# Optimization experiments

Measured on AMD Instinct MI355X. Metric: run time of the kernel, lower is better.

The kernel has to match this reference:

```python
import jax, jax.numpy as jnp
import numpy as np

DIM = 1024; N_LAYERS = 4; N_HEADS = 16; HEAD_DIM = DIM // N_HEADS
HIDDEN = 2816; VOCAB = 256; EPS = 1e-5; THETA = 10000.0
B, S = 1, 2048


def _rmsnorm(x, w):
    xf = x.astype(jnp.float32)
    n = xf * jax.lax.rsqrt(jnp.mean(xf * xf, axis=-1, keepdims=True) + EPS)
    return n.astype(x.dtype) * w


def _rope(x, cos, sin):
    # x: [B,S,H,hd]; torch view_as_complex pairs consecutive elements (0,1),(2,3),...
    xr = x[..., 0::2].astype(jnp.float32)
    xi = x[..., 1::2].astype(jnp.float32)
    c = cos[None, :, None, :]
    s = sin[None, :, None, :]
    outr = xr * c - xi * s
    outi = xr * s + xi * c
    out = jnp.stack([outr, outi], axis=-1).reshape(x.shape)
    return out.astype(x.dtype)


def setup_inputs() -> dict:
    key = jax.random.key(0)
    ks = jax.random.split(key, 10)
    std = 0.02
    def w(k, shape):
        return jax.random.normal(k, shape, jnp.float32) * std
    return {
        "tokens": jax.random.randint(ks[0], (B, S), 0, VOCAB, dtype=jnp.int32),
        "tok_emb": w(ks[1], (VOCAB, DIM)),
        "wq": w(ks[2], (N_LAYERS, DIM, DIM)),
        "wk": w(ks[3], (N_LAYERS, DIM, DIM)),
        "wv": w(ks[4], (N_LAYERS, DIM, DIM)),
        "wo": w(ks[5], (N_LAYERS, DIM, DIM)),
        "w1": w(ks[6], (N_LAYERS, HIDDEN, DIM)),
        "w2": w(ks[7], (N_LAYERS, DIM, HIDDEN)),
        "w3": w(ks[8], (N_LAYERS, HIDDEN, DIM)),
        "attn_norm_w": jnp.ones((N_LAYERS, DIM), jnp.float32),
        "ffn_norm_w": jnp.ones((N_LAYERS, DIM), jnp.float32),
        "final_norm_w": jnp.ones((DIM,), jnp.float32),
        "out_w": w(ks[9], (VOCAB, DIM)),
    }


def reference(tokens, tok_emb, wq, wk, wv, wo, w1, w2, w3,
              attn_norm_w, ffn_norm_w, final_norm_w, out_w):
    seqlen = tokens.shape[1]
    # precompute_freqs_cis
    inv = 1.0 / (THETA ** (jnp.arange(0, HEAD_DIM, 2, dtype=jnp.float32) / HEAD_DIM))
    t = jnp.arange(seqlen, dtype=jnp.float32)
    freqs = jnp.outer(t, inv)          # [S, hd/2]
    cos, sin = jnp.cos(freqs), jnp.sin(freqs)
    scale = 1.0 / np.sqrt(HEAD_DIM)

    h = tok_emb[tokens]                # [B,S,D]

    def block(h, p):
        lwq, lwk, lwv, lwo, lw1, lw2, lw3, anw, fnw = p
        x = _rmsnorm(h, anw)
        q = (x @ lwq.T).reshape(B, seqlen, N_HEADS, HEAD_DIM)
        k = (x @ lwk.T).reshape(B, seqlen, N_HEADS, HEAD_DIM)
        v = (x @ lwv.T).reshape(B, seqlen, N_HEADS, HEAD_DIM)
        q = _rope(q, cos, sin)
        k = _rope(k, cos, sin)
        # non-causal full attention (eval mode: no diffusion mask, no dropout)
        scores = jnp.einsum('bqhd,bkhd->bhqk', q, k) * scale
        probs = jax.nn.softmax(scores, axis=-1)
        attn = jnp.einsum('bhqk,bkhd->bqhd', probs, v).reshape(B, seqlen, DIM)
        h = h + attn @ lwo.T
        x = _rmsnorm(h, fnw)
        ff = (jax.nn.silu(x @ lw1.T) * (x @ lw3.T)) @ lw2.T
        return h + ff, None

    h, _ = jax.lax.scan(block, h, (wq, wk, wv, wo, w1, w2, w3, attn_norm_w, ffn_norm_w))
    h = _rmsnorm(h, final_norm_w)
    # targets=None path: logits only for the last position
    return h[:, -1:, :] @ out_w.T      # [B,1,VOCAB]
```

## Files before the change

### kernel.cpp

```cpp
#include <hip/hip_runtime.h>
#include <stdint.h>

typedef __bf16 bf16;
typedef __bf16 bf16x4 __attribute__((ext_vector_type(4)));
typedef __bf16 bf16x8 __attribute__((ext_vector_type(8)));
typedef float f32x4 __attribute__((ext_vector_type(4)));
typedef float f32x16 __attribute__((ext_vector_type(16)));

#define SEQ 2048
#define DIM 1024
#define NHEAD 16
#define HDIM 64
#define HID 2816
#define NLAYER 4

__device__ __forceinline__ void gload_lds16(const void* g, void* l) {
  __builtin_amdgcn_global_load_lds(
      (const __attribute__((address_space(1))) void*)g,
      (__attribute__((address_space(3))) void*)l, 16, 0, 0);
}

template <int MODE, int BM, int BN>
__global__ __launch_bounds__(256) void gemm_bt(
    const bf16* __restrict__ A, const bf16* __restrict__ B,
    bf16* __restrict__ Cb, float* __restrict__ Cf, const float* R,
    int M, int N, int K)
{
  constexpr int MR = BM / 32;
  constexpr int NR = BN / 32;
  constexpr int LA = BM / 64;
  constexpr int LB = BN / 64;
  __shared__ bf16 As[2 * BM * 32];
  __shared__ bf16 Bs[2 * BN * 32];
  const int tid  = threadIdx.x;
  const int wv   = tid >> 6;
  const int lane = tid & 63;
  const int lo = lane & 15, hi = lane >> 4;
  const int row0 = blockIdx.y * BM;
  const int col0 = blockIdx.x * BN;
  const int wr = (wv >> 1) * (BM / 2);
  const int wc = (wv & 1) * (BN / 2);

  f32x4 acc[MR][NR];
  const f32x4 zero = {0.f, 0.f, 0.f, 0.f};
#pragma unroll
  for (int m = 0; m < MR; ++m)
#pragma unroll
    for (int n = 0; n < NR; ++n) acc[m][n] = zero;

  const bf16* ag = A + (size_t)(row0 + (tid >> 2)) * K + (tid & 3) * 8;
  const bf16* bg = B + (size_t)(col0 + (tid >> 2)) * K + (tid & 3) * 8;

  auto stage = [&](int buf, int k) {
#pragma unroll
    for (int i = 0; i < LA; ++i)
      gload_lds16(ag + k + (size_t)i*64*K, &As[buf*BM*32 + i*2048 + wv*512]);
#pragma unroll
    for (int i = 0; i < LB; ++i)
      gload_lds16(bg + k + (size_t)i*64*K, &Bs[buf*BN*32 + i*2048 + wv*512]);
  };
  auto compute = [&](int buf) {
    bf16x8 af[MR], bfv[NR];
#pragma unroll
    for (int m = 0; m < MR; ++m)
      af[m] = *(const bf16x8*)&As[buf*BM*32 + (wr + m*16 + lo)*32 + hi*8];
#pragma unroll
    for (int n = 0; n < NR; ++n)
      bfv[n] = *(const bf16x8*)&Bs[buf*BN*32 + (wc + n*16 + lo)*32 + hi*8];
#pragma unroll
    for (int m = 0; m < MR; ++m)
#pragma unroll
      for (int n = 0; n < NR; ++n)
        acc[m][n] = __builtin_amdgcn_mfma_f32_16x16x32_bf16(af[m], bfv[n], acc[m][n], 0, 0, 0);
  };

  stage(0, 0);
  __syncthreads();
  for (int k0 = 0; k0 < K; k0 += 64) {
    stage(1, k0 + 32);
    compute(0);
    __syncthreads();
    if (k0 + 64 < K) stage(0, k0 + 64);
    compute(1);
    __syncthreads();
  }

  if (MODE == 2) {
    const int hstride = N >> 1;
#pragma unroll
    for (int m = 0; m < MR; ++m)
#pragma unroll
      for (int p = 0; p < NR/2; ++p)
#pragma unroll
        for (int r = 0; r < 4; ++r) {
          const int row  = row0 + wr + m * 16 + hi * 4 + r;
          const int hcol = (col0 + wc)/2 + p * 16 + lo;
          float u = acc[m][2*p][r], g = acc[m][2*p+1][r];
          float y = u / (1.f + __expf(-u)) * g;
          Cb[(size_t)row * hstride + hcol] = (bf16)y;
        }
  } else {
#pragma unroll
    for (int m = 0; m < MR; ++m)
#pragma unroll
      for (int n = 0; n < NR; ++n)
#pragma unroll
        for (int r = 0; r < 4; ++r) {
          const int row = row0 + wr + m * 16 + hi * 4 + r;
          const int col = col0 + wc + n * 16 + lo;
          const size_t idx = (size_t)row * N + col;
          if (MODE == 0) Cb[idx] = (bf16)acc[m][n][r];
          else           Cf[idx] = R[idx] + acc[m][n][r];
        }
  }
}

__device__ __forceinline__ void softmax_pv(
    f32x16& s, float& m, float& lsum, f32x16& o0, f32x16& o1,
    const bf16x8 (&vf)[2][2], int h)
{
  float mx = s[0];
#pragma unroll
  for (int r = 1; r < 16; ++r) mx = fmaxf(mx, s[r]);
  mx = fmaxf(mx, __shfl_xor(mx, 32));
  if (!__all(mx <= m + 11.5416f)) {
    float mnew = fmaxf(m, mx);
    float corr = __builtin_amdgcn_exp2f(m - mnew);
    m = mnew; lsum *= corr;
#pragma unroll
    for (int r = 0; r < 16; ++r) { o0[r] *= corr; o1[r] *= corr; }
  }
  float p[16]; float ps = 0.f;
#pragma unroll
  for (int r = 0; r < 16; ++r) { p[r] = __builtin_amdgcn_exp2f(s[r] - m); ps += p[r]; }
  ps += __shfl_xor(ps, 32);
  lsum += ps;

  unsigned int w[4][2];
#pragma unroll
  for (int g = 0; g < 4; ++g)
#pragma unroll
    for (int t2 = 0; t2 < 2; ++t2) {
      union { bf16 b[2]; unsigned int u; } pk;
      pk.b[0] = (bf16)p[g*4 + 2*t2];
      pk.b[1] = (bf16)p[g*4 + 2*t2 + 1];
      w[g][t2] = pk.u;
    }

#pragma unroll
  for (int c = 0; c < 2; ++c) {
    unsigned int keep0 = h ? w[2*c+1][0] : w[2*c][0];
    unsigned int keep1 = h ? w[2*c+1][1] : w[2*c][1];
    unsigned int send0 = h ? w[2*c][0]   : w[2*c+1][0];
    unsigned int send1 = h ? w[2*c][1]   : w[2*c+1][1];
    unsigned int r0 = __shfl_xor(send0, 32);
    unsigned int r1 = __shfl_xor(send1, 32);
    union { unsigned int u[4]; bf16x8 v; } pf;
    pf.u[0] = h ? r0 : keep0;
    pf.u[1] = h ? r1 : keep1;
    pf.u[2] = h ? keep0 : r0;
    pf.u[3] = h ? keep1 : r1;
    __builtin_amdgcn_s_setprio(1);
    o0 = __builtin_amdgcn_mfma_f32_32x32x16_bf16(vf[c][0], pf.v, o0, 0, 0, 0);
    o1 = __builtin_amdgcn_mfma_f32_32x32x16_bf16(vf[c][1], pf.v, o1, 0, 0, 0);
    __builtin_amdgcn_s_setprio(0);
  }
}

__device__ __forceinline__ void attn_tile64(
    const bf16* __restrict__ kb, const bf16* __restrict__ vb,
    const bf16x8 (&qfA)[4], const bf16x8 (&qfB)[4],
    bf16x8 (&kc)[4], bf16x8 (&kn)[4],
    f32x16& oA0, f32x16& oA1, f32x16& oB0, f32x16& oB1,
    float& mA, float& lA, float& mB, float& lB,
    int j0, int jn, int q5, int h)
{
  bf16x8 vf[2][2];
#pragma unroll
  for (int c = 0; c < 2; ++c)
#pragma unroll
    for (int dh = 0; dh < 2; ++dh)
      vf[c][dh] = *(const bf16x8*)&vb[(size_t)(dh*32 + q5)*2048 + j0 + c*16];
  {
    const bf16* kp = kb + (size_t)(jn + q5)*3072;
#pragma unroll
    for (int dc = 0; dc < 4; ++dc) kn[dc] = *(const bf16x8*)(kp + dc*16);
  }
  f32x16 sA, sB;
#pragma unroll
  for (int r = 0; r < 16; ++r) { sA[r] = 0.f; sB[r] = 0.f; }
  __builtin_amdgcn_s_setprio(1);
#pragma unroll
  for (int dc = 0; dc < 4; ++dc) {
    sA = __builtin_amdgcn_mfma_f32_32x32x16_bf16(kc[dc], qfA[dc], sA, 0, 0, 0);
    sB = __builtin_amdgcn_mfma_f32_32x32x16_bf16(kc[dc], qfB[dc], sB, 0, 0, 0);
  }
  __builtin_amdgcn_s_setprio(0);

  softmax_pv(sA, mA, lA, oA0, oA1, vf, h);
  softmax_pv(sB, mB, lB, oB0, oB1, vf, h);
}

__global__ __launch_bounds__(256, 2) void attn_kernel(const bf16* __restrict__ qkv,
    const bf16* __restrict__ vt, bf16* __restrict__ outb)
{
  __shared__ float Osh[4][32][65];
  __shared__ float msh[4][32];
  __shared__ float lsh[4][32];

  const int tid = threadIdx.x;
  const int wv = tid >> 6;
  const int lane = tid & 63;
  const int q5 = lane & 31, h = lane >> 5;
  const int hh = blockIdx.x;
  const int q0 = blockIdx.y * 64;

  bf16x8 qfA[4], qfB[4];
#pragma unroll
  for (int dc = 0; dc < 4; ++dc) {
    bf16x8 xa = *(const bf16x8*)&qkv[(size_t)(q0 + q5)*3072      + hh*64 + h*8 + dc*16];
    bf16x8 xb = *(const bf16x8*)&qkv[(size_t)(q0 + 32 + q5)*3072 + hh*64 + h*8 + dc*16];
#pragma unroll
    for (int j = 0; j < 8; ++j) {
      xa[j] = (bf16)(0.18033688f * (float)xa[j]);
      xb[j] = (bf16)(0.18033688f * (float)xb[j]);
    }
    qfA[dc] = xa; qfB[dc] = xb;
  }

  const bf16* kb = qkv + 1024 + hh*64 + h*8;
  const bf16* vb = vt + (size_t)hh*64*2048 + h*8;

  f32x16 oA0, oA1, oB0, oB1;
#pragma unroll
  for (int r = 0; r < 16; ++r) { oA0[r]=0.f; oA1[r]=0.f; oB0[r]=0.f; oB1[r]=0.f; }
  float mA = -1e30f, lA = 0.f, mB = -1e30f, lB = 0.f;

  bf16x8 ka[4], ka2[4];
  {
    const bf16* kp = kb + (size_t)(wv*32 + q5)*3072;
#pragma unroll
    for (int dc = 0; dc < 4; ++dc) ka[dc] = *(const bf16x8*)(kp + dc*16);
  }

  for (int t = 0; t < 16; t += 2) {
    attn_tile64(kb, vb, qfA, qfB, ka, ka2, oA0, oA1, oB0, oB1,
                mA, lA, mB, lB,
                (wv + 4*t)*32,     ((wv + 4*(t+1)) & 63)*32, q5, h);
    attn_tile64(kb, vb, qfA, qfB, ka2, ka, oA0, oA1, oB0, oB1,
                mA, lA, mB, lB,
                (wv + 4*(t+1))*32, ((wv + 4*(t+2)) & 63)*32, q5, h);
  }

  const int q = tid >> 3, d0 = (tid & 7) * 8;
#pragma unroll
  for (int pass = 0; pass < 2; ++pass) {
    const f32x16& p0 = pass ? oB0 : oA0;
    const f32x16& p1 = pass ? oB1 : oA1;
#pragma unroll
    for (int r = 0; r < 16; ++r) {
      const int dr = (r & 3) + 8*(r >> 2) + 4*h;
      Osh[wv][q5][dr]      = p0[r];
      Osh[wv][q5][32 + dr] = p1[r];
    }
    if (h == 0) {
      msh[wv][q5] = pass ? mB : mA;
      lsh[wv][q5] = pass ? lB : lA;
    }
    __syncthreads();
    {
      float mm = fmaxf(fmaxf(msh[0][q], msh[1][q]), fmaxf(msh[2][q], msh[3][q]));
      float e0 = __builtin_amdgcn_exp2f(msh[0][q] - mm),
            e1 = __builtin_amdgcn_exp2f(msh[1][q] - mm),
            e2 = __builtin_amdgcn_exp2f(msh[2][q] - mm),
            e3 = __builtin_amdgcn_exp2f(msh[3][q] - mm);
      float L = e0*lsh[0][q] + e1*lsh[1][q] + e2*lsh[2][q] + e3*lsh[3][q];
      float rinv = 1.0f / L;
      bf16x8 outv;
#pragma unroll
      for (int j = 0; j < 8; ++j) {
        float sum = e0*Osh[0][q][d0+j] + e1*Osh[1][q][d0+j]
                  + e2*Osh[2][q][d0+j] + e3*Osh[3][q][d0+j];
        outv[j] = (bf16)(sum * rinv);
      }
      *(bf16x8*)&outb[(size_t)(q0 + pass*32 + q)*DIM + hh*64 + d0] = outv;
    }
    __syncthreads();
  }
}

__global__ __launch_bounds__(256) void rope_init_kernel(float* __restrict__ ct, float* __restrict__ st) {
  int idx = blockIdx.x * 256 + threadIdx.x;
  if (idx >= SEQ * 32) return;
  int s = idx >> 5, i = idx & 31;
  float inv = powf(10000.0f, -(float)i / 32.0f);
  float f = (float)s * inv;
  ct[idx] = cosf(f);
  st[idx] = sinf(f);
}

__global__ __launch_bounds__(256) void cast_kernel(const float* __restrict__ src,
    bf16* __restrict__ dst, int perLayer, int dstStride, int dstOff, int L)
{
  int i = blockIdx.x * 256 + threadIdx.x;
  int e = i * 4;
  if (e >= perLayer * L) return;
  int l = e / perLayer;
  int o = e - l * perLayer;
  float4 v = *(const float4*)(src + e);
  bf16x4 b;
  b[0] = (bf16)v.x; b[1] = (bf16)v.y; b[2] = (bf16)v.z; b[3] = (bf16)v.w;
  *(bf16x4*)(dst + (size_t)l * dstStride + dstOff + o) = b;
}

__global__ __launch_bounds__(256) void cast_interleave_kernel(const float* __restrict__ src,
    bf16* __restrict__ dst, int isW3)
{
  const int PLh = HID * DIM;
  int i = blockIdx.x * 256 + threadIdx.x;
  int e = i * 4;
  if (e >= PLh * NLAYER) return;
  int l = e / PLh;
  int rem = e - l * PLh;
  int r = rem >> 10, c = rem & 1023;
  int dr = (r >> 4) * 32 + (isW3 ? 16 : 0) + (r & 15);
  float4 v = *(const float4*)(src + e);
  bf16x4 b;
  b[0] = (bf16)v.x; b[1] = (bf16)v.y; b[2] = (bf16)v.z; b[3] = (bf16)v.w;
  *(bf16x4*)(dst + (size_t)l * 2 * PLh + (size_t)dr * 1024 + c) = b;
}

__global__ __launch_bounds__(256) void embed_kernel(const int* __restrict__ tok,
    const float* __restrict__ emb, float* __restrict__ h)
{
  int s = blockIdx.x, t = threadIdx.x;
  int v = tok[s];
  ((float4*)(h + (size_t)s * DIM))[t] = ((const float4*)(emb + (size_t)v * DIM))[t];
}

__global__ __launch_bounds__(256) void rmsnorm_kernel(const float* __restrict__ h,
    const float* __restrict__ w, bf16* __restrict__ outb)
{
  int row = blockIdx.x, tid = threadIdx.x;
  float4 v = ((const float4*)(h + (size_t)row * DIM))[tid];
  float ss = v.x*v.x + v.y*v.y + v.z*v.z + v.w*v.w;
#pragma unroll
  for (int off = 1; off < 64; off <<= 1) ss += __shfl_xor(ss, off);
  __shared__ float red[4];
  if ((tid & 63) == 0) red[tid >> 6] = ss;
  __syncthreads();
  float tot = red[0] + red[1] + red[2] + red[3];
  float inv = rsqrtf(tot * (1.0f / DIM) + 1e-5f);
  float4 wv4 = ((const float4*)w)[tid];
  bf16x4 o;
  o[0] = (bf16)(v.x * inv * wv4.x);
  o[1] = (bf16)(v.y * inv * wv4.y);
  o[2] = (bf16)(v.z * inv * wv4.z);
  o[3] = (bf16)(v.w * inv * wv4.w);
  ((bf16x4*)(outb + (size_t)row * DIM))[tid] = o;
}

__global__ __launch_bounds__(256) void final_rms_kernel(const float* __restrict__ hrow,
    const float* __restrict__ w, float* __restrict__ fl)
{
  int tid = threadIdx.x;
  float4 v = ((const float4*)hrow)[tid];
  float ss = v.x*v.x + v.y*v.y + v.z*v.z + v.w*v.w;
#pragma unroll
  for (int off = 1; off < 64; off <<= 1) ss += __shfl_xor(ss, off);
  __shared__ float red[4];
  if ((tid & 63) == 0) red[tid >> 6] = ss;
  __syncthreads();
  float tot = red[0] + red[1] + red[2] + red[3];
  float inv = rsqrtf(tot * (1.0f / DIM) + 1e-5f);
  float4 wv4 = ((const float4*)w)[tid];
  float4 o;
  o.x = v.x * inv * wv4.x;
  o.y = v.y * inv * wv4.y;
  o.z = v.z * inv * wv4.z;
  o.w = v.w * inv * wv4.w;
  ((float4*)fl)[tid] = o;
}

__global__ __launch_bounds__(256) void rope_kernel(bf16* __restrict__ qkv,
    const float* __restrict__ ct, const float* __restrict__ st)
{
  int idx = blockIdx.x * 256 + threadIdx.x;
  if (idx >= SEQ * 128) return;
  int s = idx >> 7, rem = idx & 127;
  int h = rem >> 3, c8 = rem & 7;
  int d0 = c8 * 8, i0 = c8 * 4;
  float4 cv = *(const float4*)&ct[s*32 + i0];
  float4 sv = *(const float4*)&st[s*32 + i0];
  float c[4]  = {cv.x, cv.y, cv.z, cv.w};
  float sn[4] = {sv.x, sv.y, sv.z, sv.w};
  size_t base = (size_t)s * 3072 + h * 64 + d0;
#pragma unroll
  for (int part = 0; part < 2; ++part) {
    bf16x8 x = *(bf16x8*)&qkv[base + part * 1024];
    bf16x8 o;
#pragma unroll
    for (int p = 0; p < 4; ++p) {
      float xr = (float)x[2*p], xi = (float)x[2*p+1];
      o[2*p]   = (bf16)(xr * c[p] - xi * sn[p]);
      o[2*p+1] = (bf16)(xr * sn[p] + xi * c[p]);
    }
    *(bf16x8*)&qkv[base + part * 1024] = o;
  }
}

__global__ __launch_bounds__(256) void vtrans_kernel(const bf16* __restrict__ qkv,
    bf16* __restrict__ vt)
{
  __shared__ unsigned short T[64][66];
  const int tj = blockIdx.x & 31;
  const int td = blockIdx.x >> 5;
  const int t = threadIdx.x;
  {
    const int j = t >> 2, d0 = (t & 3) * 16;
    const bf16* src = qkv + (size_t)(tj*64 + j)*3072 + 2048 + td*64 + d0;
    bf16x8 a = *(const bf16x8*)src;
    bf16x8 b = *(const bf16x8*)(src + 8);
    union { bf16 v; unsigned short u; } cv;
#pragma unroll
    for (int i = 0; i < 8; ++i) {
      cv.v = a[i]; T[j][d0 + i] = cv.u;
      cv.v = b[i]; T[j][d0 + 8 + i] = cv.u;
    }
  }
  __syncthreads();
  {
    const int d = t >> 2, j0 = (t & 3) * 16;
    union { bf16x8 v; unsigned short u[8]; } oa, ob;
#pragma unroll
    for (int i = 0; i < 8; ++i) {
      oa.u[i] = T[j0 + i][d];
      ob.u[i] = T[j0 + 8 + i][d];
    }
    bf16* dst = vt + (size_t)(td*64 + d)*2048 + tj*64 + j0;
    *(bf16x8*)dst = oa.v;
    *(bf16x8*)(dst + 8) = ob.v;
  }
}

__global__ __launch_bounds__(64) void logits_kernel(const float* __restrict__ fl,
    const float* __restrict__ ow, float* __restrict__ outp)
{
  int v = blockIdx.x, lane = threadIdx.x;
  const float* row = ow + (size_t)v * DIM;
  float s = 0.f;
#pragma unroll
  for (int t = 0; t < 16; ++t) {
    int d = t * 64 + lane;
    s += fl[d] * row[d];
  }
#pragma unroll
  for (int off = 1; off < 64; off <<= 1) s += __shfl_xor(s, off);
  if (lane == 0) outp[v] = s;
}

extern "C" void kernel_launch(void* const* d_in, const int* in_sizes, int n_in,
                              void* d_out, int out_size, void* d_ws, size_t ws_size,
                              hipStream_t stream)
{
  const int*   tokens = (const int*)  d_in[0];
  const float* temb   = (const float*)d_in[1];
  const float* wq  = (const float*)d_in[2];
  const float* wk  = (const float*)d_in[3];
  const float* wvv = (const float*)d_in[4];
  const float* wo  = (const float*)d_in[5];
  const float* w1  = (const float*)d_in[6];
  const float* w2  = (const float*)d_in[7];
  const float* w3  = (const float*)d_in[8];
  const float* anw = (const float*)d_in[9];
  const float* fnw = (const float*)d_in[10];
  const float* finw= (const float*)d_in[11];
  const float* outw= (const float*)d_in[12];
  float* out = (float*)d_out;

  char* wsp = (char*)d_ws;
  size_t off = 0;
  auto take = [&](size_t bytes) -> void* {
    void* r = wsp + off;
    off += (bytes + 255) & ~(size_t)255;
    return r;
  };
  bf16* wqkv = (bf16*)take((size_t)NLAYER * 3072 * DIM * 2);
  bf16* wob  = (bf16*)take((size_t)NLAYER * DIM * DIM * 2);
  bf16* w13  = (bf16*)take((size_t)NLAYER * 2 * HID * DIM * 2);
  bf16* w2b  = (bf16*)take((size_t)NLAYER * DIM * HID * 2);
  float* h   = (float*)take((size_t)SEQ * DIM * 4);
  bf16* xn   = (bf16*)take((size_t)SEQ * DIM * 2);
  bf16* qkvb = (bf16*)take((size_t)SEQ * 3072 * 2);
  bf16* vtb  = (bf16*)take((size_t)DIM * SEQ * 2);
  bf16* attnb= (bf16*)take((size_t)SEQ * DIM * 2);
  bf16* hbb  = (bf16*)take((size_t)SEQ * HID * 2);
  float* ct  = (float*)take((size_t)SEQ * 32 * 4);
  float* st  = (float*)take((size_t)SEQ * 32 * 4);
  float* fl  = (float*)take((size_t)DIM * 4);

  rope_init_kernel<<<SEQ * 32 / 256, 256, 0, stream>>>(ct, st);

  const int PLd = DIM * DIM;
  const int PLh = HID * DIM;
  cast_kernel<<<PLd * NLAYER / 1024, 256, 0, stream>>>(wq,  wqkv, PLd, 3 * PLd, 0,       NLAYER);
  cast_kernel<<<PLd * NLAYER / 1024, 256, 0, stream>>>(wk,  wqkv, PLd, 3 * PLd, PLd,     NLAYER);
  cast_kernel<<<PLd * NLAYER / 1024, 256, 0, stream>>>(wvv, wqkv, PLd, 3 * PLd, 2 * PLd, NLAYER);
  cast_kernel<<<PLd * NLAYER / 1024, 256, 0, stream>>>(wo,  wob,  PLd, PLd,     0,       NLAYER);
  cast_interleave_kernel<<<PLh * NLAYER / 1024, 256, 0, stream>>>(w1, w13, 0);
  cast_interleave_kernel<<<PLh * NLAYER / 1024, 256, 0, stream>>>(w3, w13, 1);
  cast_kernel<<<PLh * NLAYER / 1024, 256, 0, stream>>>(w2,  w2b,  PLh, PLh,     0,       NLAYER);

  embed_kernel<<<SEQ, 256, 0, stream>>>(tokens, temb, h);

  for (int l = 0; l < NLAYER; ++l) {
    const bf16* lwqkv = wqkv + (size_t)l * 3 * PLd;
    const bf16* lwo   = wob  + (size_t)l * PLd;
    const bf16* lw13  = w13  + (size_t)l * 2 * PLh;
    const bf16* lw2   = w2b  + (size_t)l * PLh;

    rmsnorm_kernel<<<SEQ, 256, 0, stream>>>(h, anw + l * DIM, xn);
    gemm_bt<0,128,64><<<dim3(48, 16), 256, 0, stream>>>(xn, lwqkv, qkvb, nullptr, nullptr, SEQ, 3072, DIM);
    rope_kernel<<<SEQ * 128 / 256, 256, 0, stream>>>(qkvb, ct, st);
    vtrans_kernel<<<512, 256, 0, stream>>>(qkvb, vtb);
    attn_kernel<<<dim3(16, 32), 256, 0, stream>>>(qkvb, vtb, attnb);
    gemm_bt<1,64,64><<<dim3(16, 32), 256, 0, stream>>>(attnb, lwo, nullptr, h, h, SEQ, DIM, DIM);
    rmsnorm_kernel<<<SEQ, 256, 0, stream>>>(h, fnw + l * DIM, xn);
    gemm_bt<2,128,64><<<dim3(88, 16), 256, 0, stream>>>(xn, lw13, hbb, nullptr, nullptr, SEQ, 2 * HID, DIM);
    gemm_bt<1,64,64><<<dim3(16, 32), 256, 0, stream>>>(hbb, lw2, nullptr, h, h, SEQ, DIM, HID);
  }

  final_rms_kernel<<<1, 256, 0, stream>>>(h + (size_t)(SEQ - 1) * DIM, finw, fl);
  logits_kernel<<<256, 64, 0, stream>>>(fl, outw, out);
}
```

Measured before the change: 774.5 us.

## Fuse RoPE into QKV GEMM epilogue, merge weight casts, enlarge GEMM tiles

Adds a GEMM epilogue mode that applies rotary embedding to the Q and K columns, getting each element's pair partner with a lane shuffle, and drops the separate rope kernel and its read-modify-write pass over the QKV buffer. The five plain weight-cast launches are merged into a single kernel. The QKV and W1/W3 GEMMs move from 128x64 to 128x128 tiles, which doubles accumulator registers and halves the grid size. The rope epilogue reads cos/sin per element from global memory, and the bigger tiles may lower occupancy or leave CUs idle with fewer blocks.

```diff
diff --git a/kernel.cpp b/kernel.cpp
--- a/kernel.cpp
+++ b/kernel.cpp
@@ -24,6 +24,7 @@
 __global__ __launch_bounds__(256) void gemm_bt(
     const bf16* __restrict__ A, const bf16* __restrict__ B,
     bf16* __restrict__ Cb, float* __restrict__ Cf, const float* R,
+    const float* __restrict__ CT, const float* __restrict__ ST,
     int M, int N, int K)
 {
   constexpr int MR = BM / 32;
@@ -99,6 +100,29 @@
           float y = u / (1.f + __expf(-u)) * g;
           Cb[(size_t)row * hstride + hcol] = (bf16)y;
         }
+  } else if (MODE == 3) {
+#pragma unroll
+    for (int m = 0; m < MR; ++m)
+#pragma unroll
+      for (int n = 0; n < NR; ++n) {
+        const int col = col0 + wc + n * 16 + lo;
+        const bool qk = col < 2048;
+        const int i = (col & 63) >> 1;
+        const float sgn = (col & 1) ? 1.f : -1.f;
+#pragma unroll
+        for (int r = 0; r < 4; ++r) {
+          const int row = row0 + wr + m * 16 + hi * 4 + r;
+          float a = acc[m][n][r];
+          float partner = __shfl_xor(a, 1);
+          float outv = a;
+          if (qk) {
+            float c  = CT[row * 32 + i];
+            float sn = ST[row * 32 + i];
+            outv = a * c + sgn * partner * sn;
+          }
+          Cb[(size_t)row * N + col] = (bf16)outv;
+        }
+      }
   } else {
 #pragma unroll
     for (int m = 0; m < MR; ++m)
@@ -299,18 +323,29 @@
   st[idx] = sinf(f);
 }
 
-__global__ __launch_bounds__(256) void cast_kernel(const float* __restrict__ src,
-    bf16* __restrict__ dst, int perLayer, int dstStride, int dstOff, int L)
-{
-  int i = blockIdx.x * 256 + threadIdx.x;
-  int e = i * 4;
-  if (e >= perLayer * L) return;
-  int l = e / perLayer;
-  int o = e - l * perLayer;
-  float4 v = *(const float4*)(src + e);
+__global__ __launch_bounds__(256) void cast_all_kernel(
+    const float* __restrict__ wq, const float* __restrict__ wk,
+    const float* __restrict__ wv, const float* __restrict__ wo,
+    const float* __restrict__ w2,
+    bf16* __restrict__ wqkv, bf16* __restrict__ wob, bf16* __restrict__ w2b)
+{
+  const long long PLd = (long long)DIM * DIM;
+  const long long PLh = (long long)HID * DIM;
+  const long long S = PLd * NLAYER;
+  long long e = ((long long)blockIdx.x * 256 + threadIdx.x) * 4;
+  const float* src;
+  bf16* dst;
+  long long e2;
+  if (e < S)            { e2 = e;       src = wq; long long l = e2 / PLd, o = e2 - l*PLd; dst = wqkv + l*3*PLd + o; }
+  else if (e < 2*S)     { e2 = e - S;   src = wk; long long l = e2 / PLd, o = e2 - l*PLd; dst = wqkv + l*3*PLd + PLd + o; }
+  else if (e < 3*S)     { e2 = e - 2*S; src = wv; long long l = e2 / PLd, o = e2 - l*PLd; dst = wqkv + l*3*PLd + 2*PLd + o; }
+  else if (e < 4*S)     { e2 = e - 3*S; src = wo; dst = wob + e2; }
+  else if (e < 4*S + PLh*NLAYER) { e2 = e - 4*S; src = w2; dst = w2b + e2; }
+  else return;
+  float4 v = *(const float4*)(src + e2);
   bf16x4 b;
   b[0] = (bf16)v.x; b[1] = (bf16)v.y; b[2] = (bf16)v.z; b[3] = (bf16)v.w;
-  *(bf16x4*)(dst + (size_t)l * dstStride + dstOff + o) = b;
+  *(bf16x4*)dst = b;
 }
 
 __global__ __launch_bounds__(256) void cast_interleave_kernel(const float* __restrict__ src,
@@ -380,33 +415,6 @@
   o.z = v.z * inv * wv4.z;
   o.w = v.w * inv * wv4.w;
   ((float4*)fl)[tid] = o;
-}
-
-__global__ __launch_bounds__(256) void rope_kernel(bf16* __restrict__ qkv,
-    const float* __restrict__ ct, const float* __restrict__ st)
-{
-  int idx = blockIdx.x * 256 + threadIdx.x;
-  if (idx >= SEQ * 128) return;
-  int s = idx >> 7, rem = idx & 127;
-  int h = rem >> 3, c8 = rem & 7;
-  int d0 = c8 * 8, i0 = c8 * 4;
-  float4 cv = *(const float4*)&ct[s*32 + i0];
-  float4 sv = *(const float4*)&st[s*32 + i0];
-  float c[4]  = {cv.x, cv.y, cv.z, cv.w};
-  float sn[4] = {sv.x, sv.y, sv.z, sv.w};
-  size_t base = (size_t)s * 3072 + h * 64 + d0;
-#pragma unroll
-  for (int part = 0; part < 2; ++part) {
-    bf16x8 x = *(bf16x8*)&qkv[base + part * 1024];
-    bf16x8 o;
-#pragma unroll
-    for (int p = 0; p < 4; ++p) {
-      float xr = (float)x[2*p], xi = (float)x[2*p+1];
-      o[2*p]   = (bf16)(xr * c[p] - xi * sn[p]);
-      o[2*p+1] = (bf16)(xr * sn[p] + xi * c[p]);
-    }
-    *(bf16x8*)&qkv[base + part * 1024] = o;
-  }
 }
 
 __global__ __launch_bounds__(256) void vtrans_kernel(const bf16* __restrict__ qkv,
@@ -501,15 +509,15 @@
 
   rope_init_kernel<<<SEQ * 32 / 256, 256, 0, stream>>>(ct, st);
 
-  const int PLd = DIM * DIM;
-  const int PLh = HID * DIM;
-  cast_kernel<<<PLd * NLAYER / 1024, 256, 0, stream>>>(wq,  wqkv, PLd, 3 * PLd, 0,       NLAYER);
-  cast_kernel<<<PLd * NLAYER / 1024, 256, 0, stream>>>(wk,  wqkv, PLd, 3 * PLd, PLd,     NLAYER);
-  cast_kernel<<<PLd * NLAYER / 1024, 256, 0, stream>>>(wvv, wqkv, PLd, 3 * PLd, 2 * PLd, NLAYER);
-  cast_kernel<<<PLd * NLAYER / 1024, 256, 0, stream>>>(wo,  wob,  PLd, PLd,     0,       NLAYER);
-  cast_interleave_kernel<<<PLh * NLAYER / 1024, 256, 0, stream>>>(w1, w13, 0);
-  cast_interleave_kernel<<<PLh * NLAYER / 1024, 256, 0, stream>>>(w3, w13, 1);
-  cast_kernel<<<PLh * NLAYER / 1024, 256, 0, stream>>>(w2,  w2b,  PLh, PLh,     0,       NLAYER);
+  const long long PLd = (long long)DIM * DIM;
+  const long long PLh = (long long)HID * DIM;
+  {
+    long long totalElems = 4 * PLd * NLAYER + PLh * NLAYER;
+    int blocks = (int)((totalElems / 4 + 255) / 256);
+    cast_all_kernel<<<blocks, 256, 0, stream>>>(wq, wk, wvv, wo, w2, wqkv, wob, w2b);
+  }
+  cast_interleave_kernel<<<(int)(PLh * NLAYER / 1024), 256, 0, stream>>>(w1, w13, 0);
+  cast_interleave_kernel<<<(int)(PLh * NLAYER / 1024), 256, 0, stream>>>(w3, w13, 1);
 
   embed_kernel<<<SEQ, 256, 0, stream>>>(tokens, temb, h);
 
@@ -520,14 +528,13 @@
     const bf16* lw2   = w2b  + (size_t)l * PLh;
 
     rmsnorm_kernel<<<SEQ, 256, 0, stream>>>(h, anw + l * DIM, xn);
-    gemm_bt<0,128,64><<<dim3(48, 16), 256, 0, stream>>>(xn, lwqkv, qkvb, nullptr, nullptr, SEQ, 3072, DIM);
-    rope_kernel<<<SEQ * 128 / 256, 256, 0, stream>>>(qkvb, ct, st);
+    gemm_bt<3,128,128><<<dim3(24, 16), 256, 0, stream>>>(xn, lwqkv, qkvb, nullptr, nullptr, ct, st, SEQ, 3072, DIM);
     vtrans_kernel<<<512, 256, 0, stream>>>(qkvb, vtb);
     attn_kernel<<<dim3(16, 32), 256, 0, stream>>>(qkvb, vtb, attnb);
-    gemm_bt<1,64,64><<<dim3(16, 32), 256, 0, stream>>>(attnb, lwo, nullptr, h, h, SEQ, DIM, DIM);
+    gemm_bt<1,64,64><<<dim3(16, 32), 256, 0, stream>>>(attnb, lwo, nullptr, h, h, nullptr, nullptr, SEQ, DIM, DIM);
     rmsnorm_kernel<<<SEQ, 256, 0, stream>>>(h, fnw + l * DIM, xn);
-    gemm_bt<2,128,64><<<dim3(88, 16), 256, 0, stream>>>(xn, lw13, hbb, nullptr, nullptr, SEQ, 2 * HID, DIM);
-    gemm_bt<1,64,64><<<dim3(16, 32), 256, 0, stream>>>(hbb, lw2, nullptr, h, h, SEQ, DIM, HID);
+    gemm_bt<2,128,128><<<dim3(44, 16), 256, 0, stream>>>(xn, lw13, hbb, nullptr, nullptr, nullptr, nullptr, SEQ, 2 * HID, DIM);
+    gemm_bt<1,64,64><<<dim3(16, 32), 256, 0, stream>>>(hbb, lw2, nullptr, h, h, nullptr, nullptr, SEQ, DIM, HID);
   }
 
   final_rms_kernel<<<1, 256, 0, stream>>>(h + (size_t)(SEQ - 1) * DIM, finw, fl);
```

Measured after the change: 753.4 us. 2.7% less time.
